# Performance work log

Measured on AMD Instinct MI355X. Metric: run time of the kernel, lower is better.

The kernel has to match this reference:

```python
import jax, jax.numpy as jnp
import numpy as np

B, N, D_IN, D_OUT, NHOP = 16, 1024, 128, 128, 3


def setup_inputs() -> dict:
    key = jax.random.key(0)
    ks = jax.random.split(key, 7)
    x = jax.random.normal(ks[0], (B, N, D_IN), dtype=jnp.float32)
    # sparse-ish binary adjacency (float, as in the torch model) with self loops
    adj = (jax.random.uniform(ks[1], (B, N, N)) < 0.05).astype(jnp.float32)
    adj = jnp.maximum(adj, jnp.eye(N, dtype=jnp.float32)[None])
    # learned params (torch nn.Linear default-ish init scale)
    s_in = 1.0 / np.sqrt(D_IN)
    s_out = 1.0 / np.sqrt(2 * D_OUT)
    W_w = jax.random.uniform(ks[2], (D_OUT, D_IN), minval=-s_in, maxval=s_in, dtype=jnp.float32)
    W_b = jax.random.uniform(ks[3], (D_OUT,), minval=-s_in, maxval=s_in, dtype=jnp.float32)
    A = jax.random.normal(ks[4], (D_OUT, D_OUT), dtype=jnp.float32) * 0.02  # nn.Parameter(zeros) would kill signal; use small init
    gate_w = jax.random.uniform(ks[5], (1, 2 * D_OUT), minval=-s_out, maxval=s_out, dtype=jnp.float32)
    gate_b = jax.random.uniform(ks[6], (1,), minval=-s_out, maxval=s_out, dtype=jnp.float32)
    return {"x": x, "adj": adj, "W_w": W_w, "W_b": W_b, "A": A,
            "gate_w": gate_w, "gate_b": gate_b}


def reference(x, adj, W_w, W_b, A, gate_w, gate_b):
    # h = W(x): [B,N,D_OUT]
    h = jnp.einsum('bnd,od->bno', x, W_w) + W_b
    # bilinear score e[b,j,k] = (h A)_j . h_k, symmetrized
    e = jnp.einsum('bjl,bkl->bjk', jnp.einsum('bjd,de->bje', h, A), h)
    e = e + jnp.swapaxes(e, 1, 2)
    # masked softmax over dim=1 (as in the torch code), then re-mask
    att = jnp.where(adj > 0, e, jnp.zeros((), dtype=e.dtype))
    att = jax.nn.softmax(att, axis=1)
    att = att * adj
    retval = h
    for _ in range(NHOP):
        az = jax.nn.relu(jnp.einsum('bij,bjk->bik', att, retval))
        gate_in = jnp.concatenate([h, az], axis=-1)            # [B,N,2*D_OUT]
        coeff = jax.nn.sigmoid(jnp.einsum('bnf,of->bno', gate_in, gate_w) + gate_b)  # [B,N,1]
        retval = coeff * h + (1.0 - coeff) * az
    return retval
```

## Files before the change

### kernel.cpp

```cpp
#include <hip/hip_runtime.h>
#include <math.h>

#define Bn 16
#define Nn 1024
#define Dn 128

typedef unsigned short ushort;
typedef unsigned long long u64;
typedef short short8 __attribute__((ext_vector_type(8)));
typedef float f32x4 __attribute__((ext_vector_type(4)));
typedef ushort us8 __attribute__((ext_vector_type(8)));
typedef ushort us4 __attribute__((ext_vector_type(4)));

__device__ __forceinline__ ushort f2bf(float f) {
    unsigned u = __float_as_uint(f);
    u += 0x7fff + ((u >> 16) & 1);
    return (ushort)(u >> 16);
}
__device__ __forceinline__ float bf2f(ushort s) {
    return __uint_as_float(((unsigned)s) << 16);
}

#if defined(__has_builtin)
#if __has_builtin(__builtin_amdgcn_global_load_lds)
#define HAVE_GLL 1
#endif
#endif
#ifndef HAVE_GLL
#define HAVE_GLL 0
#endif

typedef __attribute__((address_space(1))) void as1_t;
typedef __attribute__((address_space(3))) void as3_t;

__device__ __forceinline__ void stage_group(const void* gbase, void* lbase, int lane) {
#if HAVE_GLL
    __builtin_amdgcn_global_load_lds((as1_t*)((const char*)gbase + lane * 16),
                                     (as3_t*)lbase, 16, 0, 0);
#else
    *(us8*)((char*)lbase + lane * 16) = *(const us8*)((const char*)gbase + lane * 16);
#endif
}


__global__ __launch_bounds__(256) void k_ph0(const float* __restrict__ Ww,
                                             const float* __restrict__ A,
                                             const float* __restrict__ adj,
                                             ushort* __restrict__ Whi, ushort* __restrict__ Wlo,
                                             ushort* __restrict__ Shi, ushort* __restrict__ Slo,
                                             float* __restrict__ Z, u64* __restrict__ bm) {
    int L = blockIdx.x, t = threadIdx.x;
    if (L < 64) {
        int i = L * 256 + t;
        float w = Ww[i];
        ushort wh = f2bf(w);
        Whi[i] = wh;
        Wlo[i] = f2bf(w - bf2f(wh));
        int e = i >> 7, d = i & 127;
        float s = A[i] + A[d * Dn + e];
        ushort sh = f2bf(s);
        Shi[i] = sh;
        Slo[i] = f2bf(s - bf2f(sh));
        Z[i] = (float)Nn;
    }
    int gwv = L * 4 + (t >> 6);
    int lane = t & 63;
    #pragma unroll 4
    for (int it = 0; it < 16; ++it) {
        int pair = gwv * 16 + it;
        const float* p = adj + (size_t)pair * 256 + lane * 4;
        float4 v = *(const float4*)p;
        u64 b0 = __ballot(v.x > 0.f);
        u64 b1 = __ballot(v.y > 0.f);
        u64 b2 = __ballot(v.z > 0.f);
        u64 b3 = __ballot(v.w > 0.f);
        if (lane == 0) {
            u64* d = bm + (size_t)pair * 4;
            d[0] = b0; d[1] = b1; d[2] = b2; d[3] = b3;
        }
    }
}

__global__ __launch_bounds__(256) void k_h(const float* __restrict__ x,
                                           const float* __restrict__ Wb,
                                           const ushort* __restrict__ Whi,
                                           const ushort* __restrict__ Wlo,
                                           const ushort* __restrict__ Shi,
                                           const ushort* __restrict__ Slo,
                                           float* __restrict__ h,
                                           ushort* __restrict__ h16f,
                                           ushort* __restrict__ g16f) {
    int I0 = blockIdx.x * 16;
    int t = threadIdx.x, w = t >> 6, lane = t & 63;
    int m = lane & 15, q = lane >> 4;

    __shared__ float xs[16][Dn + 4];
    __shared__ float hs[16][Dn + 4];
    __shared__ float gs_[16][Dn + 4];

    {
        int r = t >> 4, c8 = (t & 15) * 8;
        const float* src = x + (size_t)(I0 + r) * Dn + c8;
        *(float4*)&xs[r][c8]     = *(const float4*)(src);
        *(float4*)&xs[r][c8 + 4] = *(const float4*)(src + 4);
    }
    __syncthreads();

    f32x4 acc0 = {0,0,0,0}, acc1 = {0,0,0,0};
    #pragma unroll
    for (int ks = 0; ks < 4; ++ks) {
        int k0 = q * 8 + ks * 32;
        float v[8]; short8 ahi, alo;
        *(float4*)(v)     = *(const float4*)(&xs[m][k0]);
        *(float4*)(v + 4) = *(const float4*)(&xs[m][k0 + 4]);
        #pragma unroll
        for (int j = 0; j < 8; ++j) {
            ushort hi = f2bf(v[j]);
            ahi[j] = (short)hi;
            alo[j] = (short)f2bf(v[j] - bf2f(hi));
        }
        #pragma unroll
        for (int nn = 0; nn < 2; ++nn) {
            int brow = (w * 2 + nn) * 16 + m;
            short8 bhi = __builtin_bit_cast(short8, ((const us8*)(Whi + (size_t)brow * Dn))[q + ks * 4]);
            short8 blo = __builtin_bit_cast(short8, ((const us8*)(Wlo + (size_t)brow * Dn))[q + ks * 4]);
            f32x4 acc = nn ? acc1 : acc0;
            acc = __builtin_amdgcn_mfma_f32_16x16x32_bf16(ahi, bhi, acc, 0, 0, 0);
            acc = __builtin_amdgcn_mfma_f32_16x16x32_bf16(alo, bhi, acc, 0, 0, 0);
            acc = __builtin_amdgcn_mfma_f32_16x16x32_bf16(ahi, blo, acc, 0, 0, 0);
            if (nn) acc1 = acc; else acc0 = acc;
        }
    }
    #pragma unroll
    for (int nn = 0; nn < 2; ++nn) {
        int col = (w * 2 + nn) * 16 + m;
        float bias = Wb[col];
        f32x4 acc = nn ? acc1 : acc0;
        #pragma unroll
        for (int r = 0; r < 4; ++r) {
            int rl = q * 4 + r;
            float hv = acc[r] + bias;
            h[(size_t)(I0 + rl) * Dn + col] = hv;
            hs[rl][col] = hv;
        }
    }
    __syncthreads();

    f32x4 bcc0 = {0,0,0,0}, bcc1 = {0,0,0,0};
    #pragma unroll
    for (int ks = 0; ks < 4; ++ks) {
        int k0 = q * 8 + ks * 32;
        float v[8]; short8 ahi, alo;
        *(float4*)(v)     = *(const float4*)(&hs[m][k0]);
        *(float4*)(v + 4) = *(const float4*)(&hs[m][k0 + 4]);
        #pragma unroll
        for (int j = 0; j < 8; ++j) {
            ushort hi = f2bf(v[j]);
            ahi[j] = (short)hi;
            alo[j] = (short)f2bf(v[j] - bf2f(hi));
        }
        #pragma unroll
        for (int nn = 0; nn < 2; ++nn) {
            int brow = (w * 2 + nn) * 16 + m;
            short8 bhi = __builtin_bit_cast(short8, ((const us8*)(Shi + (size_t)brow * Dn))[q + ks * 4]);
            short8 blo = __builtin_bit_cast(short8, ((const us8*)(Slo + (size_t)brow * Dn))[q + ks * 4]);
            f32x4 acc = nn ? bcc1 : bcc0;
            acc = __builtin_amdgcn_mfma_f32_16x16x32_bf16(ahi, bhi, acc, 0, 0, 0);
            acc = __builtin_amdgcn_mfma_f32_16x16x32_bf16(alo, bhi, acc, 0, 0, 0);
            acc = __builtin_amdgcn_mfma_f32_16x16x32_bf16(ahi, blo, acc, 0, 0, 0);
            if (nn) bcc1 = acc; else bcc0 = acc;
        }
    }
    #pragma unroll
    for (int nn = 0; nn < 2; ++nn) {
        int col = (w * 2 + nn) * 16 + m;
        f32x4 acc = nn ? bcc1 : bcc0;
        #pragma unroll
        for (int r = 0; r < 4; ++r)
            gs_[q * 4 + r][col] = acc[r];
    }
    __syncthreads();

    {
        int kc = t >> 6, mm = (t >> 2) & 15, qq = t & 3;
        int cb = kc * 32 + qq * 8;
        us8 oh, oa;
        #pragma unroll
        for (int e = 0; e < 8; ++e) {
            oh[e] = f2bf(hs[mm][cb + e]);
            oa[e] = f2bf(gs_[mm][cb + e]);
        }
        size_t U = (size_t)(I0 >> 4) * 256 + kc * 64 + mm * 4 + qq;
        ((us8*)h16f)[U] = oh;
        ((us8*)g16f)[U] = oa;
    }
}

__global__ __launch_bounds__(256, 4) void k_scores(const ushort* __restrict__ g16f,
                                                   const ushort* __restrict__ h16f,
                                                   const u64* __restrict__ bm,
                                                   ushort* __restrict__ Ef,
                                                   float* __restrict__ Z) {
    int L = blockIdx.x;
    int b    = ((L & 7) << 1) | (L >> 11);
    int tile = (L >> 3) & 255;
    int I0 = (tile >> 4) << 6;
    int J0 = (tile & 15) << 6;
    int t = threadIdx.x, wid = t >> 6, lane = t & 63;
    int m = lane & 15, q = lane >> 4;
    int off16 = (m * 4 + q) * 16;

    __shared__ __align__(16) char smem[18432];
    float (*sc)[68] = (float(*)[68])smem;
    float (*cz)[64] = (float(*)[64])(smem + 17408);

    {
        const char* hbp = (const char*)h16f + (size_t)b * 262144;
        for (int g = wid; g < 16; g += 4) {
            int rt_l = g >> 2, kk = g & 3;
            stage_group(hbp + ((size_t)((J0 >> 4) + rt_l) * 256 + kk * 64) * 16,
                        smem + g * 1024, lane);
        }
    }
    short8 afr[4];
    {
        const char* gbp = (const char*)g16f + (size_t)b * 262144
                        + (size_t)((I0 >> 4) + wid) * 4096 + off16;
        #pragma unroll
        for (int ks = 0; ks < 4; ++ks)
            afr[ks] = __builtin_bit_cast(short8, *(const us8*)(gbp + ks * 1024));
    }
    __syncthreads();

    f32x4 acc[4] = {};
    #pragma unroll
    for (int ks = 0; ks < 4; ++ks) {
        #pragma unroll
        for (int nt = 0; nt < 4; ++nt) {
            short8 bb = __builtin_bit_cast(short8,
                *(const us8*)(smem + (nt * 4 + ks) * 1024 + off16));
            acc[nt] = __builtin_amdgcn_mfma_f32_16x16x32_bf16(afr[ks], bb, acc[nt], 0, 0, 0);
        }
    }
    __syncthreads();

    #pragma unroll
    for (int nt = 0; nt < 4; ++nt)
        #pragma unroll
        for (int r = 0; r < 4; ++r)
            sc[wid * 16 + q * 4 + r][nt * 16 + m] = acc[nt][r];
    __syncthreads();

    int row16 = t >> 4, c = t & 15;
    int bitc = ((J0 >> 2) & 63) + c;
    float colsum[4] = {0.f, 0.f, 0.f, 0.f};
    #pragma unroll
    for (int it = 0; it < 4; ++it) {
        int row = it * 16 + row16;
        const u64* wp = bm + ((size_t)(b * Nn + I0 + row) * 4 + (J0 >> 8)) * 4;
        u64 wj[4] = {wp[0], wp[1], wp[2], wp[3]};
        float s4[4];
        *(float4*)s4 = *(const float4*)(&sc[row][c * 4]);
        us4 e4;
        #pragma unroll
        for (int j = 0; j < 4; ++j) {
            float ex = __expf(s4[j]);
            bool on = (wj[j] >> bitc) & 1;
            e4[j] = f2bf(on ? ex : 0.f);
            colsum[j] += on ? (ex - 1.0f) : 0.f;
        }
        size_t U = ((((size_t)b * 64 + (I0 >> 4) + it) * 32 + (J0 >> 5) + (c >> 3)) * 16 + row16) * 4
                 + ((c & 7) >> 1);
        *(us4*)(Ef + U * 8 + (c & 1) * 4) = e4;
    }
    #pragma unroll
    for (int j = 0; j < 4; ++j) {
        colsum[j] += __shfl_xor(colsum[j], 16, 64);
        colsum[j] += __shfl_xor(colsum[j], 32, 64);
    }
    if (lane < 16) {
        #pragma unroll
        for (int j = 0; j < 4; ++j) cz[wid][lane * 4 + j] = colsum[j];
    }
    __syncthreads();
    if (t < 64) {
        float s = cz[0][t] + cz[1][t] + cz[2][t] + cz[3][t];
        atomicAdd(&Z[b * Nn + J0 + t], s);
    }
}

__global__ __launch_bounds__(256) void k_prep(const float* __restrict__ src,
                                              const float* __restrict__ Z,
                                              ushort* __restrict__ Tf) {
    int b = blockIdx.y;
    int j0 = blockIdx.x * 64;
    int t = threadIdx.x;
    __shared__ float ls[64][129];
    __shared__ float iz[64];
    if (t < 64) iz[t] = 1.0f / Z[b * Nn + j0 + t];
    __syncthreads();
    #pragma unroll
    for (int it = 0; it < 8; ++it) {
        int idx = it * 256 + t;
        int j = idx >> 5, k4 = (idx & 31) * 4;
        float4 v = *(const float4*)(src + ((size_t)b * Nn + j0 + j) * Dn + k4);
        float z = iz[j];
        ls[j][k4] = v.x * z; ls[j][k4 + 1] = v.y * z;
        ls[j][k4 + 2] = v.z * z; ls[j][k4 + 3] = v.w * z;
    }
    __syncthreads();
    int k = t & 127, half = t >> 7;
    us8 o[4];
    #pragma unroll
    for (int qq = 0; qq < 4; ++qq) {
        us8 tmp;
        #pragma unroll
        for (int e = 0; e < 8; ++e)
            tmp[e] = f2bf(ls[half * 32 + qq * 8 + e][k]);
        o[qq] = tmp;
    }
    size_t U = (((size_t)(k >> 4) * 32 + (j0 >> 5) + half) * 16 + (k & 15)) * 4;
    us8* dst = (us8*)(Tf + (size_t)b * 131072 + U * 8);
    dst[0] = o[0]; dst[1] = o[1]; dst[2] = o[2]; dst[3] = o[3];
}

#define STAGEB(buf, cch) do {                                                          \
    for (int g = w; g < 32; g += 4) {                                                  \
        stage_group(tfb + ((size_t)(g >> 2) * 32 + (cch) * 4 + (g & 3)) * 1024,        \
                    smem + (buf) * 32768 + g * 1024, lane);                            \
    } } while (0)

#define HOP_CHUNK(cch, CUR, NXT)                                                       \
    if ((cch) < 7) {                                                                   \
        STAGEB(((cch) + 1) & 1, (cch) + 1);                                            \
        _Pragma("unroll")                                                              \
        for (int kk = 0; kk < 4; ++kk)                                                 \
            NXT[kk] = __builtin_bit_cast(short8,                                       \
                *(const us8*)(ebase + (((cch) + 1) * 4 + kk) * 1024));                 \
    }                                                                                  \
    _Pragma("unroll")                                                                  \
    for (int kk = 0; kk < 4; ++kk) {                                                   \
        _Pragma("unroll")                                                              \
        for (int nt = 0; nt < 8; ++nt) {                                               \
            short8 bf = __builtin_bit_cast(short8,                                     \
                *(const us8*)(smem + ((cch) & 1) * 32768 + (nt * 4 + kk) * 1024 + off16)); \
            acc[nt] = __builtin_amdgcn_mfma_f32_16x16x32_bf16(CUR[kk], bf, acc[nt], 0, 0, 0); \
        }                                                                              \
    }                                                                                  \
    __syncthreads();

__global__ __launch_bounds__(256, 1) void k_hop(const ushort* __restrict__ Ef,
                                                const ushort* __restrict__ Tf,
                                                const float* __restrict__ h,
                                                const float* __restrict__ Z,
                                                const float* __restrict__ gw,
                                                const float* __restrict__ gb,
                                                ushort* __restrict__ Tfn,
                                                float* __restrict__ out,
                                                int last) {
    int L = blockIdx.x;
    int b  = ((L & 7) << 1) | (L >> 7);
    int t4 = (L >> 3) & 15;
    int t = threadIdx.x, w = t >> 6, lane = t & 63;
    int m = lane & 15, q = lane >> 4;
    int rt = t4 * 4 + w;
    int I0 = rt << 4;

    __shared__ __align__(16) char smem[65536];
    int off16 = (m * 4 + q) * 16;

    const char* tfb   = (const char*)Tf + (size_t)b * 262144;
    const char* ebase = (const char*)Ef + (size_t)(b * 64 + rt) * 32768 + off16;

    f32x4 acc[8] = {};
    short8 aA[4], aB[4];

    STAGEB(0, 0);
    #pragma unroll
    for (int kk = 0; kk < 4; ++kk)
        aA[kk] = __builtin_bit_cast(short8, *(const us8*)(ebase + kk * 1024));
    __syncthreads();

    HOP_CHUNK(0, aA, aB)
    HOP_CHUNK(1, aB, aA)
    HOP_CHUNK(2, aA, aB)
    HOP_CHUNK(3, aB, aA)
    HOP_CHUNK(4, aA, aB)
    HOP_CHUNK(5, aB, aA)
    HOP_CHUNK(6, aA, aB)
    HOP_CHUNK(7, aB, aA)

    float gb0 = gb[0];
    float gwa[8], gwz[8];
    #pragma unroll
    for (int nt = 0; nt < 8; ++nt) { gwa[nt] = gw[nt * 16 + m]; gwz[nt] = gw[Dn + nt * 16 + m]; }

    float hv[8][4], coef[4];
    size_t hbase = ((size_t)b * Nn + I0) * Dn;
    #pragma unroll
    for (int r = 0; r < 4; ++r) {
        int row = q * 4 + r;
        float gs = 0.f;
        #pragma unroll
        for (int nt = 0; nt < 8; ++nt) {
            float az = fmaxf(acc[nt][r], 0.f);
            acc[nt][r] = az;
            float hh = h[hbase + (size_t)row * Dn + nt * 16 + m];
            hv[nt][r] = hh;
            gs += hh * gwa[nt] + az * gwz[nt];
        }
        gs += __shfl_xor(gs, 1, 64);
        gs += __shfl_xor(gs, 2, 64);
        gs += __shfl_xor(gs, 4, 64);
        gs += __shfl_xor(gs, 8, 64);
        coef[r] = 1.0f / (1.0f + __expf(-(gs + gb0)));
    }

    if (last) {
        #pragma unroll
        for (int r = 0; r < 4; ++r) {
            int row = q * 4 + r;
            float cc = coef[r];
            #pragma unroll
            for (int nt = 0; nt < 8; ++nt)
                out[hbase + (size_t)row * Dn + nt * 16 + m] =
                    cc * hv[nt][r] + (1.f - cc) * acc[nt][r];
        }
    } else {
        ushort (*tt)[128][16] = (ushort(*)[128][16])smem;
        #pragma unroll
        for (int r = 0; r < 4; ++r) {
            int row = q * 4 + r;
            float cc = coef[r];
            float iz = 1.0f / Z[b * Nn + I0 + row];
            #pragma unroll
            for (int nt = 0; nt < 8; ++nt) {
                float v = cc * hv[nt][r] + (1.f - cc) * acc[nt][r];
                tt[w][nt * 16 + m][row] = f2bf(v * iz);
            }
        }
        __syncthreads();
        int k = t >> 1, jh = t & 1;
        size_t U0 = (((size_t)(k >> 4) * 32 + t4 * 2 + jh) * 16 + (k & 15)) * 4;
        ushort* dst = Tfn + (size_t)b * 131072 + U0 * 8;
        #pragma unroll
        for (int qq = 0; qq < 4; ++qq)
            *(us8*)(dst + qq * 8) = *(const us8*)&tt[jh * 2 + (qq >> 1)][k][(qq & 1) * 8];
    }
}

extern "C" void kernel_launch(void* const* d_in, const int* in_sizes, int n_in,
                              void* d_out, int out_size, void* d_ws, size_t ws_size,
                              hipStream_t stream) {
    const float* x    = (const float*)d_in[0];
    const float* adj  = (const float*)d_in[1];
    const float* Ww   = (const float*)d_in[2];
    const float* Wb   = (const float*)d_in[3];
    const float* A    = (const float*)d_in[4];
    const float* gw   = (const float*)d_in[5];
    const float* gb   = (const float*)d_in[6];
    float* out = (float*)d_out;

    char* ws = (char*)d_ws;
    float*  h    = (float*)(ws);
    ushort* Ta   = (ushort*)(ws + (8u << 20));
    ushort* Tb   = (ushort*)(ws + (12u << 20));
    ushort* E    = (ushort*)(ws + (16u << 20));
    float*  Z    = (float*)(ws + (48u << 20));
    ushort* Whi  = (ushort*)(ws + (48u << 20) + (64u << 10));
    ushort* Wlo  = (ushort*)(ws + (48u << 20) + (96u << 10));
    ushort* Shi  = (ushort*)(ws + (48u << 20) + (128u << 10));
    ushort* Slo  = (ushort*)(ws + (48u << 20) + (160u << 10));
    u64*    bm   = (u64*)(ws + (48u << 20) + (192u << 10));

    k_ph0   <<<1024, 256, 0, stream>>>(Ww, A, adj, Whi, Wlo, Shi, Slo, Z, bm);
    k_h     <<<1024, 256, 0, stream>>>(x, Wb, Whi, Wlo, Shi, Slo, h, Ta, Tb);
    k_scores<<<4096, 256, 0, stream>>>(Tb, Ta, bm, E, Z);
    k_prep  <<<dim3(16, Bn), 256, 0, stream>>>(h, Z, Ta);
    k_hop   <<<256, 256, 0, stream>>>(E, Ta, h, Z, gw, gb, Tb, out, 0);
    k_hop   <<<256, 256, 0, stream>>>(E, Tb, h, Z, gw, gb, Ta, out, 0);
    k_hop   <<<256, 256, 0, stream>>>(E, Ta, h, Z, gw, gb, (ushort*)nullptr, out, 1);
}
```

Before: 198.2 us.

## Triple-buffer hop kernel staging with vmcnt waits and lane-contiguous fragment layout

Changes the packed bf16 fragment layout so each lane's 16-byte MFMA operand sits at lane*16, making fragment loads contiguous across the wavefront. The producers (k_proj output, k_scores E writes, k_prep, and the hop's next-T writes) are updated to match. The hop kernel moves from a double-buffered loop with full __syncthreads to a three-stage LDS pipeline (96KB shared) that uses explicit s_waitcnt vmcnt plus s_barrier. This keeps two chunks of loads in flight while the MFMAs run. The costs are more LDS per block and fragile hand-counted vmcnt values that depend on how many loads stage_group issues.

```diff
diff --git a/kernel.cpp b/kernel.cpp
--- a/kernel.cpp
+++ b/kernel.cpp
@@ -190,7 +190,7 @@
             oh[e] = f2bf(hs[mm][cb + e]);
             oa[e] = f2bf(gs_[mm][cb + e]);
         }
-        size_t U = (size_t)(I0 >> 4) * 256 + kc * 64 + mm * 4 + qq;
+        size_t U = (size_t)(I0 >> 4) * 256 + kc * 64 + qq * 16 + mm;
         ((us8*)h16f)[U] = oh;
         ((us8*)g16f)[U] = oa;
     }
@@ -207,8 +207,7 @@
     int I0 = (tile >> 4) << 6;
     int J0 = (tile & 15) << 6;
     int t = threadIdx.x, wid = t >> 6, lane = t & 63;
-    int m = lane & 15, q = lane >> 4;
-    int off16 = (m * 4 + q) * 16;
+    int loff = lane * 16;
 
     __shared__ __align__(16) char smem[18432];
     float (*sc)[68] = (float(*)[68])smem;
@@ -225,7 +224,7 @@
     short8 afr[4];
     {
         const char* gbp = (const char*)g16f + (size_t)b * 262144
-                        + (size_t)((I0 >> 4) + wid) * 4096 + off16;
+                        + (size_t)((I0 >> 4) + wid) * 4096 + loff;
         #pragma unroll
         for (int ks = 0; ks < 4; ++ks)
             afr[ks] = __builtin_bit_cast(short8, *(const us8*)(gbp + ks * 1024));
@@ -238,17 +237,20 @@
         #pragma unroll
         for (int nt = 0; nt < 4; ++nt) {
             short8 bb = __builtin_bit_cast(short8,
-                *(const us8*)(smem + (nt * 4 + ks) * 1024 + off16));
+                *(const us8*)(smem + (nt * 4 + ks) * 1024 + loff));
             acc[nt] = __builtin_amdgcn_mfma_f32_16x16x32_bf16(afr[ks], bb, acc[nt], 0, 0, 0);
         }
     }
     __syncthreads();
 
-    #pragma unroll
-    for (int nt = 0; nt < 4; ++nt)
-        #pragma unroll
-        for (int r = 0; r < 4; ++r)
-            sc[wid * 16 + q * 4 + r][nt * 16 + m] = acc[nt][r];
+    {
+        int m = lane & 15, q = lane >> 4;
+        #pragma unroll
+        for (int nt = 0; nt < 4; ++nt)
+            #pragma unroll
+            for (int r = 0; r < 4; ++r)
+                sc[wid * 16 + q * 4 + r][nt * 16 + m] = acc[nt][r];
+    }
     __syncthreads();
 
     int row16 = t >> 4, c = t & 15;
@@ -269,9 +271,9 @@
             e4[j] = f2bf(on ? ex : 0.f);
             colsum[j] += on ? (ex - 1.0f) : 0.f;
         }
-        size_t U = ((((size_t)b * 64 + (I0 >> 4) + it) * 32 + (J0 >> 5) + (c >> 3)) * 16 + row16) * 4
-                 + ((c & 7) >> 1);
-        *(us4*)(Ef + U * 8 + (c & 1) * 4) = e4;
+        size_t base = ((((size_t)b * 64 + (I0 >> 4) + it) * 32 + (J0 >> 5) + (c >> 3)) * 512)
+                    + (size_t)((c & 7) >> 1) * 128 + row16 * 8 + (c & 1) * 4;
+        *(us4*)(Ef + base) = e4;
     }
     #pragma unroll
     for (int j = 0; j < 4; ++j) {
@@ -319,35 +321,42 @@
             tmp[e] = f2bf(ls[half * 32 + qq * 8 + e][k]);
         o[qq] = tmp;
     }
-    size_t U = (((size_t)(k >> 4) * 32 + (j0 >> 5) + half) * 16 + (k & 15)) * 4;
-    us8* dst = (us8*)(Tf + (size_t)b * 131072 + U * 8);
-    dst[0] = o[0]; dst[1] = o[1]; dst[2] = o[2]; dst[3] = o[3];
-}
-
-#define STAGEB(buf, cch) do {                                                          \
-    for (int g = w; g < 32; g += 4) {                                                  \
+    size_t G = (size_t)(k >> 4) * 32 + (j0 >> 5) + half;
+    ushort* dst = Tf + (size_t)b * 131072 + G * 512 + (size_t)(k & 15) * 8;
+    #pragma unroll
+    for (int qq = 0; qq < 4; ++qq)
+        *(us8*)(dst + qq * 128) = o[qq];
+}
+
+#define STAGEB(BUF, cch) do {                                                          \
+    for (int g = w; g < 32; g += 4)                                                    \
         stage_group(tfb + ((size_t)(g >> 2) * 32 + (cch) * 4 + (g & 3)) * 1024,        \
-                    smem + (buf) * 32768 + g * 1024, lane);                            \
-    } } while (0)
-
-#define HOP_CHUNK(cch, CUR, NXT)                                                       \
-    if ((cch) < 7) {                                                                   \
-        STAGEB(((cch) + 1) & 1, (cch) + 1);                                            \
-        _Pragma("unroll")                                                              \
-        for (int kk = 0; kk < 4; ++kk)                                                 \
-            NXT[kk] = __builtin_bit_cast(short8,                                       \
-                *(const us8*)(ebase + (((cch) + 1) * 4 + kk) * 1024));                 \
-    }                                                                                  \
+                    smem + (BUF) * 32768 + g * 1024, lane);                            \
+} while (0)
+
+#define ELOAD(SET, cch) do {                                                           \
+    _Pragma("unroll")                                                                  \
+    for (int kk = 0; kk < 4; ++kk)                                                     \
+        SET[kk] = __builtin_bit_cast(short8,                                           \
+            *(const us8*)(ebase + ((cch) * 4 + kk) * 1024));                           \
+} while (0)
+
+#define MFMAC(BUF, SET) do {                                                           \
     _Pragma("unroll")                                                                  \
     for (int kk = 0; kk < 4; ++kk) {                                                   \
         _Pragma("unroll")                                                              \
         for (int nt = 0; nt < 8; ++nt) {                                               \
             short8 bf = __builtin_bit_cast(short8,                                     \
-                *(const us8*)(smem + ((cch) & 1) * 32768 + (nt * 4 + kk) * 1024 + off16)); \
-            acc[nt] = __builtin_amdgcn_mfma_f32_16x16x32_bf16(CUR[kk], bf, acc[nt], 0, 0, 0); \
+                *(const us8*)(smem + (BUF) * 32768 + (nt * 4 + kk) * 1024 + loff));    \
+            acc[nt] = __builtin_amdgcn_mfma_f32_16x16x32_bf16(SET[kk], bf, acc[nt], 0, 0, 0); \
         }                                                                              \
     }                                                                                  \
-    __syncthreads();
+} while (0)
+
+#define WAITB(NC) do {                                                                 \
+    asm volatile("s_waitcnt vmcnt(" #NC ")" ::: "memory");                             \
+    __builtin_amdgcn_s_barrier();                                                      \
+} while (0)
 
 __global__ __launch_bounds__(256, 1) void k_hop(const ushort* __restrict__ Ef,
                                                 const ushort* __restrict__ Tf,
@@ -365,30 +374,26 @@
     int m = lane & 15, q = lane >> 4;
     int rt = t4 * 4 + w;
     int I0 = rt << 4;
-
-    __shared__ __align__(16) char smem[65536];
-    int off16 = (m * 4 + q) * 16;
-
+    int loff = lane * 16;
+
+    __shared__ __align__(16) char smem[98304];
     const char* tfb   = (const char*)Tf + (size_t)b * 262144;
-    const char* ebase = (const char*)Ef + (size_t)(b * 64 + rt) * 32768 + off16;
+    const char* ebase = (const char*)Ef + (size_t)(b * 64 + rt) * 32768 + loff;
 
     f32x4 acc[8] = {};
-    short8 aA[4], aB[4];
-
-    STAGEB(0, 0);
-    #pragma unroll
-    for (int kk = 0; kk < 4; ++kk)
-        aA[kk] = __builtin_bit_cast(short8, *(const us8*)(ebase + kk * 1024));
-    __syncthreads();
-
-    HOP_CHUNK(0, aA, aB)
-    HOP_CHUNK(1, aB, aA)
-    HOP_CHUNK(2, aA, aB)
-    HOP_CHUNK(3, aB, aA)
-    HOP_CHUNK(4, aA, aB)
-    HOP_CHUNK(5, aB, aA)
-    HOP_CHUNK(6, aA, aB)
-    HOP_CHUNK(7, aB, aA)
+    short8 aA[4], aB[4], aC[4];
+
+    STAGEB(0, 0); ELOAD(aA, 0);
+    STAGEB(1, 1); ELOAD(aB, 1);
+
+    WAITB(16); STAGEB(2, 2); ELOAD(aC, 2); MFMAC(0, aA);
+    WAITB(16); STAGEB(0, 3); ELOAD(aA, 3); MFMAC(1, aB);
+    WAITB(16); STAGEB(1, 4); ELOAD(aB, 4); MFMAC(2, aC);
+    WAITB(16); STAGEB(2, 5); ELOAD(aC, 5); MFMAC(0, aA);
+    WAITB(16); STAGEB(0, 6); ELOAD(aA, 6); MFMAC(1, aB);
+    WAITB(16); STAGEB(1, 7); ELOAD(aB, 7); MFMAC(2, aC);
+    WAITB(16);                             MFMAC(0, aA);
+    WAITB(4);                              MFMAC(1, aB);
 
     float gb0 = gb[0];
     float gwa[8], gwz[8];
@@ -441,11 +446,11 @@
         }
         __syncthreads();
         int k = t >> 1, jh = t & 1;
-        size_t U0 = (((size_t)(k >> 4) * 32 + t4 * 2 + jh) * 16 + (k & 15)) * 4;
-        ushort* dst = Tfn + (size_t)b * 131072 + U0 * 8;
+        size_t G = (size_t)(k >> 4) * 32 + t4 * 2 + jh;
+        ushort* dst = Tfn + (size_t)b * 131072 + G * 512 + (size_t)(k & 15) * 8;
         #pragma unroll
         for (int qq = 0; qq < 4; ++qq)
-            *(us8*)(dst + qq * 8) = *(const us8*)&tt[jh * 2 + (qq >> 1)][k][(qq & 1) * 8];
+            *(us8*)(dst + qq * 128) = *(const us8*)&tt[jh * 2 + (qq >> 1)][k][(qq & 1) * 8];
     }
 }
 
```

After: 193.2 us. 1.03x faster.
